# Performance work log

Measured on AMD Instinct MI355X. Metric: run time of the kernel, lower is better.

## Reference

```python
import jax, jax.numpy as jnp
import numpy as np

B, T, D, S, K = 4, 4096, 1024, 2048, 4
LN_EPS = 1e-5


def setup_inputs() -> dict:
    key = jax.random.key(0)
    ks = jax.random.split(key, 9)
    scale = 0.02
    return {
        "x": jax.random.normal(ks[0], (B, T, D), jnp.float32),
        "W_in": jax.random.normal(ks[1], (D, 2 * S), jnp.float32) * scale,
        "b_in": jnp.zeros((2 * S,), jnp.float32),
        "conv_w": jax.random.normal(ks[2], (S, 1, K), jnp.float32) * scale,  # depthwise [out_ch, in_ch/groups=1, K]
        "conv_b": jnp.zeros((S,), jnp.float32),
        "W_out": jax.random.normal(ks[3], (S, D), jnp.float32) * scale,
        "b_out": jnp.zeros((D,), jnp.float32),
        "gamma": jnp.ones((D,), jnp.float32),
        "beta": jnp.zeros((D,), jnp.float32),
    }


def reference(x, W_in, b_in, conv_w, conv_b, W_out, b_out, gamma, beta):
    # x: [B, T, D]
    residual = x
    proj = x @ W_in + b_in                      # [B, T, 2S]
    mixed, gate = jnp.split(proj, 2, axis=-1)   # each [B, T, S]
    mixed = mixed * jax.nn.sigmoid(gate)
    h = jnp.transpose(mixed, (0, 2, 1))         # [B, S, T]
    k = conv_w.shape[-1]
    # torch pads both sides by K-1 then slices [:T] -> equivalent to causal left-pad K-1
    y = jax.lax.conv_general_dilated(
        h, conv_w,
        window_strides=(1,),
        padding=[(k - 1, 0)],
        dimension_numbers=("NCH", "OIH", "NCH"),
        feature_group_count=conv_w.shape[0],
    ) + conv_b[None, :, None]                   # [B, S, T]
    y = jnp.transpose(y, (0, 2, 1))             # [B, T, S]
    y = y @ W_out + b_out                       # [B, T, D]
    z = residual + y                            # dropout p=0.0 -> identity
    mu = jnp.mean(z, axis=-1, keepdims=True)
    var = jnp.var(z, axis=-1, keepdims=True)
    zn = (z - mu) * jax.lax.rsqrt(var + LN_EPS)
    return zn * gamma + beta
```

## Files before the change

kernel.cpp:

```cpp
#include <hip/hip_runtime.h>
#include <hip/hip_bf16.h>


#define Bdim 4
#define Tdim 4096
#define Ddim 1024
#define Sdim 2048
#define Mdim (Bdim * Tdim)
#define LN_EPS 1e-5f

typedef __bf16 bf16;
typedef __bf16 bf16x8 __attribute__((ext_vector_type(8)));
typedef float f32x4 __attribute__((ext_vector_type(4)));

__device__ __forceinline__ void gload_lds16(const bf16* g, bf16* l) {
  __builtin_amdgcn_global_load_lds((const __attribute__((address_space(1))) void*)g,
                                   (__attribute__((address_space(3))) void*)l,
                                   16, 0, 0);
}

__device__ __forceinline__ f32x4 zero4() {
  f32x4 z; z[0] = 0.f; z[1] = 0.f; z[2] = 0.f; z[3] = 0.f; return z;
}

__global__ __launch_bounds__(256) void k_cast_x(const float* __restrict__ x,
                                                bf16* __restrict__ xb) {
  int gid = blockIdx.x * 256 + threadIdx.x;
  const float4* p = (const float4*)x + (size_t)gid * 2;
  float4 a = p[0], b = p[1];
  bf16x8 o;
  o[0] = (bf16)a.x; o[1] = (bf16)a.y; o[2] = (bf16)a.z; o[3] = (bf16)a.w;
  o[4] = (bf16)b.x; o[5] = (bf16)b.y; o[6] = (bf16)b.z; o[7] = (bf16)b.w;
  ((bf16x8*)xb)[gid] = o;
}

__global__ __launch_bounds__(256) void k_transpose_cast(const float* __restrict__ in,
                                                        bf16* __restrict__ out,
                                                        int R, int C) {
  __shared__ float tile[32][33];
  int tx = threadIdx.x & 31;
  int ty = threadIdx.x >> 5;
  int r0 = blockIdx.y * 32;
  int c0 = blockIdx.x * 32;
#pragma unroll
  for (int i = 0; i < 4; ++i)
    tile[ty + i * 8][tx] = in[(size_t)(r0 + ty + i * 8) * C + c0 + tx];
  __syncthreads();
#pragma unroll
  for (int i = 0; i < 4; ++i)
    out[(size_t)(c0 + ty + i * 8) * R + r0 + tx] = (bf16)tile[tx][ty + i * 8];
}

__global__ __launch_bounds__(256, 2)
void k_gemm1_gate(const bf16* __restrict__ xb, const bf16* __restrict__ wt,
                  const float* __restrict__ b_in, bf16* __restrict__ mixed) {
  __shared__ bf16 Als[128 * 32];
  __shared__ bf16 Bml[128 * 32];
  __shared__ bf16 Bgl[128 * 32];

  const int tid = threadIdx.x;
  const int wave = tid >> 6;
  const int lane = tid & 63;
  const int lr = lane & 15;
  const int lk = lane >> 4;
  const int wr = wave >> 1, wc = wave & 1;

  const int m0 = blockIdx.y * 128;
  const int n0 = blockIdx.x * 128;

  const int srow = lane >> 2;
  const int skoff = (lane & 3) * 8;

  f32x4 accm[4][4], accg[4][4];
#pragma unroll
  for (int i = 0; i < 4; ++i)
#pragma unroll
    for (int j = 0; j < 4; ++j) { accm[i][j] = zero4(); accg[i][j] = zero4(); }

  const bf16* Ag = xb + (size_t)m0 * Ddim;
  const bf16* Bmg = wt + (size_t)n0 * Ddim;
  const bf16* Bgg = wt + (size_t)(Sdim + n0) * Ddim;

  for (int k0 = 0; k0 < Ddim; k0 += 32) {
    __syncthreads();
#pragma unroll
    for (int j = 0; j < 2; ++j) {
      int row = j * 64 + wave * 16 + srow;
      size_t goff = (size_t)row * Ddim + k0 + skoff;
      int lbase = (j * 64 + wave * 16) * 32;
      gload_lds16(Ag + goff, &Als[lbase]);
      gload_lds16(Bmg + goff, &Bml[lbase]);
      gload_lds16(Bgg + goff, &Bgl[lbase]);
    }
    __syncthreads();

    bf16x8 af[4], bmf[4], bgf[4];
#pragma unroll
    for (int mi = 0; mi < 4; ++mi)
      af[mi] = *(const bf16x8*)&Als[(wr * 64 + mi * 16 + lr) * 32 + lk * 8];
#pragma unroll
    for (int ni = 0; ni < 4; ++ni) {
      bmf[ni] = *(const bf16x8*)&Bml[(wc * 64 + ni * 16 + lr) * 32 + lk * 8];
      bgf[ni] = *(const bf16x8*)&Bgl[(wc * 64 + ni * 16 + lr) * 32 + lk * 8];
    }
#pragma unroll
    for (int mi = 0; mi < 4; ++mi)
#pragma unroll
      for (int ni = 0; ni < 4; ++ni) {
        accm[mi][ni] = __builtin_amdgcn_mfma_f32_16x16x32_bf16(af[mi], bmf[ni], accm[mi][ni], 0, 0, 0);
        accg[mi][ni] = __builtin_amdgcn_mfma_f32_16x16x32_bf16(af[mi], bgf[ni], accg[mi][ni], 0, 0, 0);
      }
  }

#pragma unroll
  for (int mi = 0; mi < 4; ++mi)
#pragma unroll
    for (int ni = 0; ni < 4; ++ni)
#pragma unroll
      for (int i = 0; i < 4; ++i) {
        int row = m0 + wr * 64 + mi * 16 + lk * 4 + i;
        int col = n0 + wc * 64 + ni * 16 + lr;
        float pm = accm[mi][ni][i] + b_in[col];
        float pg = accg[mi][ni][i] + b_in[col + Sdim];
        float v = pm / (1.0f + __expf(-pg));
        mixed[(size_t)row * Sdim + col] = (bf16)v;
      }
}

__global__ __launch_bounds__(256) void k_conv(const bf16* __restrict__ mixed,
                                              const float* __restrict__ cw,
                                              const float* __restrict__ cb,
                                              bf16* __restrict__ h) {
  int gid = blockIdx.x * 256 + threadIdx.x;
  int cg = gid & 255;
  int tg = (gid >> 8) & 511;
  int b = gid >> 17;
  int ch0 = cg * 8;
  int t0 = tg * 8;
  const size_t base = ((size_t)b * Tdim) * Sdim + ch0;

  float4 w4[8];
  float bias[8];
#pragma unroll
  for (int j = 0; j < 8; ++j) {
    w4[j] = ((const float4*)cw)[ch0 + j];
    bias[j] = cb[ch0 + j];
  }

  bf16x8 zv;
#pragma unroll
  for (int j = 0; j < 8; ++j) zv[j] = (bf16)0.0f;

  bf16x8 win[11];
#pragma unroll
  for (int i = 0; i < 11; ++i) {
    int t = t0 - 3 + i;
    win[i] = (t >= 0) ? *(const bf16x8*)(mixed + base + (size_t)t * Sdim) : zv;
  }

#pragma unroll
  for (int i = 0; i < 8; ++i) {
    bf16x8 o;
#pragma unroll
    for (int j = 0; j < 8; ++j) {
      float a = bias[j]
              + w4[j].x * (float)win[i + 0][j]
              + w4[j].y * (float)win[i + 1][j]
              + w4[j].z * (float)win[i + 2][j]
              + w4[j].w * (float)win[i + 3][j];
      o[j] = (bf16)a;
    }
    *(bf16x8*)(h + base + (size_t)(t0 + i) * Sdim) = o;
  }
}

__global__ __launch_bounds__(256, 2)
void k_gemm2_res(const bf16* __restrict__ h, const bf16* __restrict__ wt,
                 const float* __restrict__ b_out, const float* __restrict__ x,
                 float* __restrict__ z) {
  __shared__ bf16 Als[128 * 32];
  __shared__ bf16 Bls[128 * 32];

  const int tid = threadIdx.x;
  const int wave = tid >> 6;
  const int lane = tid & 63;
  const int lr = lane & 15;
  const int lk = lane >> 4;
  const int wr = wave >> 1, wc = wave & 1;

  const int m0 = blockIdx.y * 128;
  const int n0 = blockIdx.x * 128;

  const int srow = lane >> 2;
  const int skoff = (lane & 3) * 8;

  f32x4 acc[4][4];
#pragma unroll
  for (int i = 0; i < 4; ++i)
#pragma unroll
    for (int j = 0; j < 4; ++j) acc[i][j] = zero4();

  const bf16* Ag = h + (size_t)m0 * Sdim;
  const bf16* Bg = wt + (size_t)n0 * Sdim;

  for (int k0 = 0; k0 < Sdim; k0 += 32) {
    __syncthreads();
#pragma unroll
    for (int j = 0; j < 2; ++j) {
      int row = j * 64 + wave * 16 + srow;
      size_t goff = (size_t)row * Sdim + k0 + skoff;
      int lbase = (j * 64 + wave * 16) * 32;
      gload_lds16(Ag + goff, &Als[lbase]);
      gload_lds16(Bg + goff, &Bls[lbase]);
    }
    __syncthreads();

    bf16x8 af[4], bf[4];
#pragma unroll
    for (int mi = 0; mi < 4; ++mi)
      af[mi] = *(const bf16x8*)&Als[(wr * 64 + mi * 16 + lr) * 32 + lk * 8];
#pragma unroll
    for (int ni = 0; ni < 4; ++ni)
      bf[ni] = *(const bf16x8*)&Bls[(wc * 64 + ni * 16 + lr) * 32 + lk * 8];
#pragma unroll
    for (int mi = 0; mi < 4; ++mi)
#pragma unroll
      for (int ni = 0; ni < 4; ++ni)
        acc[mi][ni] = __builtin_amdgcn_mfma_f32_16x16x32_bf16(af[mi], bf[ni], acc[mi][ni], 0, 0, 0);
  }

#pragma unroll
  for (int mi = 0; mi < 4; ++mi)
#pragma unroll
    for (int ni = 0; ni < 4; ++ni)
#pragma unroll
      for (int i = 0; i < 4; ++i) {
        int row = m0 + wr * 64 + mi * 16 + lk * 4 + i;
        int col = n0 + wc * 64 + ni * 16 + lr;
        size_t idx = (size_t)row * Ddim + col;
        z[idx] = x[idx] + b_out[col] + acc[mi][ni][i];
      }
}

__global__ __launch_bounds__(256) void k_ln(const float* __restrict__ z,
                                            const float* __restrict__ gamma,
                                            const float* __restrict__ beta,
                                            float* __restrict__ out) {
  int row = blockIdx.x;
  int tid = threadIdx.x;
  const float4* zr = (const float4*)(z + (size_t)row * Ddim);
  float4 v = zr[tid];
  float s = v.x + v.y + v.z + v.w;
  float ss = v.x * v.x + v.y * v.y + v.z * v.z + v.w * v.w;
#pragma unroll
  for (int off = 32; off > 0; off >>= 1) {
    s += __shfl_xor(s, off);
    ss += __shfl_xor(ss, off);
  }
  __shared__ float ps[4], pss[4];
  int wave = tid >> 6, lane = tid & 63;
  if (lane == 0) { ps[wave] = s; pss[wave] = ss; }
  __syncthreads();
  float tots = ps[0] + ps[1] + ps[2] + ps[3];
  float totss = pss[0] + pss[1] + pss[2] + pss[3];
  float mu = tots * (1.0f / (float)Ddim);
  float var = totss * (1.0f / (float)Ddim) - mu * mu;
  float rs = rsqrtf(var + LN_EPS);
  float4 gg = ((const float4*)gamma)[tid];
  float4 bb = ((const float4*)beta)[tid];
  float4 o;
  o.x = (v.x - mu) * rs * gg.x + bb.x;
  o.y = (v.y - mu) * rs * gg.y + bb.y;
  o.z = (v.z - mu) * rs * gg.z + bb.z;
  o.w = (v.w - mu) * rs * gg.w + bb.w;
  ((float4*)(out + (size_t)row * Ddim))[tid] = o;
}

extern "C" void kernel_launch(void* const* d_in, const int* in_sizes, int n_in,
                              void* d_out, int out_size, void* d_ws, size_t ws_size,
                              hipStream_t stream) {
  const float* x = (const float*)d_in[0];
  const float* W_in = (const float*)d_in[1];
  const float* b_in = (const float*)d_in[2];
  const float* conv_w = (const float*)d_in[3];
  const float* conv_b = (const float*)d_in[4];
  const float* W_out = (const float*)d_in[5];
  const float* b_out = (const float*)d_in[6];
  const float* gamma = (const float*)d_in[7];
  const float* beta = (const float*)d_in[8];
  float* out = (float*)d_out;

  char* ws = (char*)d_ws;
  bf16* mixed = (bf16*)ws;
  bf16* hbuf = (bf16*)(ws + ((size_t)64 << 20));
  bf16* xb = (bf16*)(ws + ((size_t)128 << 20));
  bf16* winT = (bf16*)(ws + ((size_t)160 << 20));
  bf16* woutT = (bf16*)(ws + ((size_t)168 << 20));
  float* z = (float*)mixed;

  k_cast_x<<<dim3(Mdim * Ddim / 8 / 256), dim3(256), 0, stream>>>(x, xb);
  k_transpose_cast<<<dim3(4096 / 32, 1024 / 32), dim3(256), 0, stream>>>(W_in, winT, 1024, 4096);
  k_transpose_cast<<<dim3(1024 / 32, 2048 / 32), dim3(256), 0, stream>>>(W_out, woutT, 2048, 1024);
  k_gemm1_gate<<<dim3(Sdim / 128, Mdim / 128), dim3(256), 0, stream>>>(xb, winT, b_in, mixed);
  k_conv<<<dim3(Bdim * (Tdim / 8) * (Sdim / 8) / 256), dim3(256), 0, stream>>>(mixed, conv_w, conv_b, hbuf);
  k_gemm2_res<<<dim3(Ddim / 128, Mdim / 128), dim3(256), 0, stream>>>(hbuf, woutT, b_out, x, z);
  k_ln<<<dim3(Mdim), dim3(256), 0, stream>>>(z, gamma, beta, out);
}
```

Before: 443.7 us.

## Replace both GEMMs with a 256x256 double-buffered, swizzled, barrier-scheduled MFMA kernel

```diff
diff --git a/kernel.cpp b/kernel.cpp
--- a/kernel.cpp
+++ b/kernel.cpp
@@ -12,6 +12,12 @@
 typedef __bf16 bf16;
 typedef __bf16 bf16x8 __attribute__((ext_vector_type(8)));
 typedef float f32x4 __attribute__((ext_vector_type(4)));
+
+#define BAR() __builtin_amdgcn_s_barrier()
+#define SCHED() __builtin_amdgcn_sched_barrier(0)
+#define LGKM0() asm volatile("s_waitcnt lgkmcnt(0)" ::: "memory")
+#define VMCNT4() asm volatile("s_waitcnt vmcnt(4)" ::: "memory")
+#define VMCNT0() asm volatile("s_waitcnt vmcnt(0)" ::: "memory")
 
 __device__ __forceinline__ void gload_lds16(const bf16* g, bf16* l) {
   __builtin_amdgcn_global_load_lds((const __attribute__((address_space(1))) void*)g,
@@ -36,7 +42,7 @@
 
 __global__ __launch_bounds__(256) void k_transpose_cast(const float* __restrict__ in,
                                                         bf16* __restrict__ out,
-                                                        int R, int C) {
+                                                        int R, int C, int permmode) {
   __shared__ float tile[32][33];
   int tx = threadIdx.x & 31;
   int ty = threadIdx.x >> 5;
@@ -47,84 +53,191 @@
     tile[ty + i * 8][tx] = in[(size_t)(r0 + ty + i * 8) * C + c0 + tx];
   __syncthreads();
 #pragma unroll
-  for (int i = 0; i < 4; ++i)
-    out[(size_t)(c0 + ty + i * 8) * R + r0 + tx] = (bf16)tile[tx][ty + i * 8];
-}
-
-__global__ __launch_bounds__(256, 2)
-void k_gemm1_gate(const bf16* __restrict__ xb, const bf16* __restrict__ wt,
-                  const float* __restrict__ b_in, bf16* __restrict__ mixed) {
-  __shared__ bf16 Als[128 * 32];
-  __shared__ bf16 Bml[128 * 32];
-  __shared__ bf16 Bgl[128 * 32];
+  for (int i = 0; i < 4; ++i) {
+    int oc = c0 + ty + i * 8;
+    int pr = oc;
+    if (permmode) {
+      pr = (oc < 2048) ? ((oc >> 4) * 32 + (oc & 15))
+                       : (((oc - 2048) >> 4) * 32 + 16 + (oc & 15));
+    }
+    out[(size_t)pr * R + r0 + tx] = (bf16)tile[tx][ty + i * 8];
+  }
+}
+
+template<int KTOT, int NTN, int EPI>
+__global__ __launch_bounds__(512, 1)
+void k_gemm256(const bf16* __restrict__ Ag, const bf16* __restrict__ Bg,
+               const float* __restrict__ bias, const float* __restrict__ xres,
+               bf16* __restrict__ outb, float* __restrict__ outf) {
+  __shared__ __attribute__((aligned(16))) char lds[131072];
 
   const int tid = threadIdx.x;
-  const int wave = tid >> 6;
-  const int lane = tid & 63;
-  const int lr = lane & 15;
-  const int lk = lane >> 4;
-  const int wr = wave >> 1, wc = wave & 1;
-
-  const int m0 = blockIdx.y * 128;
-  const int n0 = blockIdx.x * 128;
-
-  const int srow = lane >> 2;
-  const int skoff = (lane & 3) * 8;
-
-  f32x4 accm[4][4], accg[4][4];
-#pragma unroll
-  for (int i = 0; i < 4; ++i)
-#pragma unroll
-    for (int j = 0; j < 4; ++j) { accm[i][j] = zero4(); accg[i][j] = zero4(); }
-
-  const bf16* Ag = xb + (size_t)m0 * Ddim;
-  const bf16* Bmg = wt + (size_t)n0 * Ddim;
-  const bf16* Bgg = wt + (size_t)(Sdim + n0) * Ddim;
-
-  for (int k0 = 0; k0 < Ddim; k0 += 32) {
-    __syncthreads();
-#pragma unroll
-    for (int j = 0; j < 2; ++j) {
-      int row = j * 64 + wave * 16 + srow;
-      size_t goff = (size_t)row * Ddim + k0 + skoff;
-      int lbase = (j * 64 + wave * 16) * 32;
-      gload_lds16(Ag + goff, &Als[lbase]);
-      gload_lds16(Bmg + goff, &Bml[lbase]);
-      gload_lds16(Bgg + goff, &Bgl[lbase]);
-    }
-    __syncthreads();
-
-    bf16x8 af[4], bmf[4], bgf[4];
-#pragma unroll
-    for (int mi = 0; mi < 4; ++mi)
-      af[mi] = *(const bf16x8*)&Als[(wr * 64 + mi * 16 + lr) * 32 + lk * 8];
-#pragma unroll
-    for (int ni = 0; ni < 4; ++ni) {
-      bmf[ni] = *(const bf16x8*)&Bml[(wc * 64 + ni * 16 + lr) * 32 + lk * 8];
-      bgf[ni] = *(const bf16x8*)&Bgl[(wc * 64 + ni * 16 + lr) * 32 + lk * 8];
-    }
-#pragma unroll
-    for (int mi = 0; mi < 4; ++mi)
-#pragma unroll
-      for (int ni = 0; ni < 4; ++ni) {
-        accm[mi][ni] = __builtin_amdgcn_mfma_f32_16x16x32_bf16(af[mi], bmf[ni], accm[mi][ni], 0, 0, 0);
-        accg[mi][ni] = __builtin_amdgcn_mfma_f32_16x16x32_bf16(af[mi], bgf[ni], accg[mi][ni], 0, 0, 0);
-      }
-  }
-
-#pragma unroll
-  for (int mi = 0; mi < 4; ++mi)
-#pragma unroll
-    for (int ni = 0; ni < 4; ++ni)
-#pragma unroll
-      for (int i = 0; i < 4; ++i) {
-        int row = m0 + wr * 64 + mi * 16 + lk * 4 + i;
-        int col = n0 + wc * 64 + ni * 16 + lr;
-        float pm = accm[mi][ni][i] + b_in[col];
-        float pg = accg[mi][ni][i] + b_in[col + Sdim];
-        float v = pm / (1.0f + __expf(-pg));
-        mixed[(size_t)row * Sdim + col] = (bf16)v;
-      }
+  const int w = tid >> 6, lane = tid & 63;
+  const int lr = lane & 15, lk = lane >> 4;
+  const int wr = w >> 2, wc = w & 3;
+
+  const int nwg = gridDim.x;
+  const int bid = blockIdx.x;
+  const int wg = (bid & 7) * (nwg >> 3) + (bid >> 3);
+  const int m0 = (wg / NTN) * 256;
+  const int n0 = (wg % NTN) * 256;
+
+  const int lsw = (lane * 16) ^ (((lane >> 5) & 1) << 5);
+  const int rw = lsw >> 7;
+  const int cw = (lsw & 127) >> 1;
+
+  const int xorm = ((lr >> 2) & 1) << 5;
+  const int aoff = (lr * 128 + lk * 16) ^ xorm;
+  const int boff = ((((wc & 1) * 64 + lr) * 128) + lk * 16) ^ xorm;
+  const char* ldsA = lds + wr * 16384;
+  const char* ldsB = lds + 32768 + (wc >> 1) * 16384;
+
+  auto stage = [&](const bf16* G, int row0, int kt, int regionByte) {
+#pragma unroll
+    for (int L = 0; L < 2; ++L) {
+      int q = w * 2 + L;
+      const bf16* src = G + (size_t)(row0 + q * 8 + rw) * KTOT + kt * 64 + cw;
+      gload_lds16(src, (bf16*)(lds + regionByte + q * 1024));
+    }
+  };
+  auto rdA = [&](int s, int mi, int ks) -> bf16x8 {
+    return *(const bf16x8*)(ldsA + s * 65536 + mi * 2048 + ks * 64 + aoff);
+  };
+  auto rdB = [&](int s, int nj, int ks) -> bf16x8 {
+    return *(const bf16x8*)(ldsB + s * 65536 + nj * 2048 + ks * 64 + boff);
+  };
+
+  f32x4 acc[8][4];
+#pragma unroll
+  for (int i = 0; i < 8; ++i)
+#pragma unroll
+    for (int j = 0; j < 4; ++j) acc[i][j] = zero4();
+
+  bf16x8 a[4][2], b[4][2];
+
+#define QUAD(rh, ch)                                                                   \
+  {                                                                                    \
+    _Pragma("unroll")                                                                  \
+    for (int mi = 0; mi < 4; ++mi) {                                                   \
+      _Pragma("unroll")                                                                \
+      for (int nj = 0; nj < 2; ++nj) {                                                 \
+        acc[(rh)*4+mi][(ch)*2+nj] = __builtin_amdgcn_mfma_f32_16x16x32_bf16(           \
+            a[mi][0], b[(ch)*2+nj][0], acc[(rh)*4+mi][(ch)*2+nj], 0, 0, 0);            \
+        acc[(rh)*4+mi][(ch)*2+nj] = __builtin_amdgcn_mfma_f32_16x16x32_bf16(           \
+            a[mi][1], b[(ch)*2+nj][1], acc[(rh)*4+mi][(ch)*2+nj], 0, 0, 0);            \
+      }                                                                                \
+    }                                                                                  \
+  }
+
+  const int NI = KTOT / 128;
+
+  stage(Bg, n0,       0, 32768);
+  stage(Bg, n0 + 128, 0, 32768 + 16384);
+  stage(Ag, m0,       0, 0);
+  stage(Ag, m0 + 128, 0, 16384);
+  stage(Bg, n0,       1, 65536 + 32768);
+  stage(Bg, n0 + 128, 1, 65536 + 32768 + 16384);
+  VMCNT4(); SCHED(); BAR(); SCHED();
+
+  for (int i = 0; i < NI; ++i) {
+    const int kta2 = 2 * i + 2;
+    const int ktb  = 2 * i + 1;
+    const bool nl = (i < NI - 1);
+
+#pragma unroll
+    for (int mi = 0; mi < 4; ++mi) { a[mi][0] = rdA(0, mi, 0); a[mi][1] = rdA(0, mi, 1); }
+#pragma unroll
+    for (int nj = 0; nj < 2; ++nj) { b[nj][0] = rdB(0, nj, 0); b[nj][1] = rdB(0, nj, 1); }
+    stage(Ag, m0, ktb, 65536);
+    asm volatile("s_waitcnt lgkmcnt(8)" ::: "memory");
+    SCHED(); BAR(); LGKM0(); SCHED();
+    __builtin_amdgcn_s_setprio(1); QUAD(0, 0); __builtin_amdgcn_s_setprio(0);
+    SCHED(); BAR(); SCHED();
+
+#pragma unroll
+    for (int nj = 0; nj < 2; ++nj) { b[2+nj][0] = rdB(0, 2+nj, 0); b[2+nj][1] = rdB(0, 2+nj, 1); }
+    stage(Ag, m0 + 128, ktb, 65536 + 16384);
+    SCHED(); BAR(); LGKM0(); SCHED();
+    __builtin_amdgcn_s_setprio(1); QUAD(0, 1); __builtin_amdgcn_s_setprio(0);
+    SCHED(); BAR(); SCHED();
+
+#pragma unroll
+    for (int mi = 0; mi < 4; ++mi) { a[mi][0] = rdA(0, 4+mi, 0); a[mi][1] = rdA(0, 4+mi, 1); }
+    if (nl) stage(Bg, n0, kta2, 32768);
+    SCHED(); BAR(); LGKM0(); SCHED();
+    __builtin_amdgcn_s_setprio(1); QUAD(1, 0); __builtin_amdgcn_s_setprio(0);
+    SCHED(); BAR(); SCHED();
+
+    if (nl) stage(Bg, n0 + 128, kta2, 32768 + 16384);
+    SCHED(); BAR(); LGKM0(); SCHED();
+    __builtin_amdgcn_s_setprio(1); QUAD(1, 1); __builtin_amdgcn_s_setprio(0);
+    if (nl) { VMCNT4(); } else { VMCNT0(); }
+    SCHED(); BAR(); SCHED();
+
+#pragma unroll
+    for (int mi = 0; mi < 4; ++mi) { a[mi][0] = rdA(1, mi, 0); a[mi][1] = rdA(1, mi, 1); }
+#pragma unroll
+    for (int nj = 0; nj < 2; ++nj) { b[nj][0] = rdB(1, nj, 0); b[nj][1] = rdB(1, nj, 1); }
+    if (nl) stage(Ag, m0, kta2, 0);
+    asm volatile("s_waitcnt lgkmcnt(8)" ::: "memory");
+    SCHED(); BAR(); LGKM0(); SCHED();
+    __builtin_amdgcn_s_setprio(1); QUAD(0, 0); __builtin_amdgcn_s_setprio(0);
+    SCHED(); BAR(); SCHED();
+
+#pragma unroll
+    for (int nj = 0; nj < 2; ++nj) { b[2+nj][0] = rdB(1, 2+nj, 0); b[2+nj][1] = rdB(1, 2+nj, 1); }
+    if (nl) stage(Ag, m0 + 128, kta2, 16384);
+    SCHED(); BAR(); LGKM0(); SCHED();
+    __builtin_amdgcn_s_setprio(1); QUAD(0, 1); __builtin_amdgcn_s_setprio(0);
+    SCHED(); BAR(); SCHED();
+
+#pragma unroll
+    for (int mi = 0; mi < 4; ++mi) { a[mi][0] = rdA(1, 4+mi, 0); a[mi][1] = rdA(1, 4+mi, 1); }
+    if (nl) stage(Bg, n0, ktb + 2, 65536 + 32768);
+    SCHED(); BAR(); LGKM0(); SCHED();
+    __builtin_amdgcn_s_setprio(1); QUAD(1, 0); __builtin_amdgcn_s_setprio(0);
+    SCHED(); BAR(); SCHED();
+
+    if (nl) stage(Bg, n0 + 128, ktb + 2, 65536 + 32768 + 16384);
+    SCHED(); BAR(); LGKM0(); SCHED();
+    __builtin_amdgcn_s_setprio(1); QUAD(1, 1); __builtin_amdgcn_s_setprio(0);
+    if (nl) { VMCNT4(); }
+    SCHED(); BAR(); SCHED();
+  }
+#undef QUAD
+
+  if (EPI == 0) {
+#pragma unroll
+    for (int p = 0; p < 2; ++p) {
+      const int g = (n0 + wc * 64 + p * 32) >> 5;
+      const int mcol = g * 16 + lr;
+      const float bm = bias[mcol];
+      const float bg = bias[mcol + 2048];
+#pragma unroll
+      for (int mi = 0; mi < 8; ++mi)
+#pragma unroll
+        for (int ii = 0; ii < 4; ++ii) {
+          const int row = m0 + wr * 128 + mi * 16 + lk * 4 + ii;
+          const float pm = acc[mi][2 * p][ii] + bm;
+          const float pg = acc[mi][2 * p + 1][ii] + bg;
+          outb[(size_t)row * Sdim + mcol] = (bf16)(pm / (1.0f + __expf(-pg)));
+        }
+    }
+  } else {
+#pragma unroll
+    for (int nj = 0; nj < 4; ++nj) {
+      const int col = n0 + wc * 64 + nj * 16 + lr;
+      const float bo = bias[col];
+#pragma unroll
+      for (int mi = 0; mi < 8; ++mi)
+#pragma unroll
+        for (int ii = 0; ii < 4; ++ii) {
+          const int row = m0 + wr * 128 + mi * 16 + lk * 4 + ii;
+          const size_t idx = (size_t)row * Ddim + col;
+          outf[idx] = xres[idx] + bo + acc[mi][nj][ii];
+        }
+    }
+  }
 }
 
 __global__ __launch_bounds__(256) void k_conv(const bf16* __restrict__ mixed,
@@ -134,10 +247,10 @@
   int gid = blockIdx.x * 256 + threadIdx.x;
   int cg = gid & 255;
   int tg = (gid >> 8) & 511;
-  int b = gid >> 17;
+  int bb = gid >> 17;
   int ch0 = cg * 8;
   int t0 = tg * 8;
-  const size_t base = ((size_t)b * Tdim) * Sdim + ch0;
+  const size_t base = ((size_t)bb * Tdim) * Sdim + ch0;
 
   float4 w4[8];
   float bias[8];
@@ -163,83 +276,15 @@
     bf16x8 o;
 #pragma unroll
     for (int j = 0; j < 8; ++j) {
-      float a = bias[j]
+      float aa = bias[j]
               + w4[j].x * (float)win[i + 0][j]
               + w4[j].y * (float)win[i + 1][j]
               + w4[j].z * (float)win[i + 2][j]
               + w4[j].w * (float)win[i + 3][j];
-      o[j] = (bf16)a;
+      o[j] = (bf16)aa;
     }
     *(bf16x8*)(h + base + (size_t)(t0 + i) * Sdim) = o;
   }
-}
-
-__global__ __launch_bounds__(256, 2)
-void k_gemm2_res(const bf16* __restrict__ h, const bf16* __restrict__ wt,
-                 const float* __restrict__ b_out, const float* __restrict__ x,
-                 float* __restrict__ z) {
-  __shared__ bf16 Als[128 * 32];
-  __shared__ bf16 Bls[128 * 32];
-
-  const int tid = threadIdx.x;
-  const int wave = tid >> 6;
-  const int lane = tid & 63;
-  const int lr = lane & 15;
-  const int lk = lane >> 4;
-  const int wr = wave >> 1, wc = wave & 1;
-
-  const int m0 = blockIdx.y * 128;
-  const int n0 = blockIdx.x * 128;
-
-  const int srow = lane >> 2;
-  const int skoff = (lane & 3) * 8;
-
-  f32x4 acc[4][4];
-#pragma unroll
-  for (int i = 0; i < 4; ++i)
-#pragma unroll
-    for (int j = 0; j < 4; ++j) acc[i][j] = zero4();
-
-  const bf16* Ag = h + (size_t)m0 * Sdim;
-  const bf16* Bg = wt + (size_t)n0 * Sdim;
-
-  for (int k0 = 0; k0 < Sdim; k0 += 32) {
-    __syncthreads();
-#pragma unroll
-    for (int j = 0; j < 2; ++j) {
-      int row = j * 64 + wave * 16 + srow;
-      size_t goff = (size_t)row * Sdim + k0 + skoff;
-      int lbase = (j * 64 + wave * 16) * 32;
-      gload_lds16(Ag + goff, &Als[lbase]);
-      gload_lds16(Bg + goff, &Bls[lbase]);
-    }
-    __syncthreads();
-
-    bf16x8 af[4], bf[4];
-#pragma unroll
-    for (int mi = 0; mi < 4; ++mi)
-      af[mi] = *(const bf16x8*)&Als[(wr * 64 + mi * 16 + lr) * 32 + lk * 8];
-#pragma unroll
-    for (int ni = 0; ni < 4; ++ni)
-      bf[ni] = *(const bf16x8*)&Bls[(wc * 64 + ni * 16 + lr) * 32 + lk * 8];
-#pragma unroll
-    for (int mi = 0; mi < 4; ++mi)
-#pragma unroll
-      for (int ni = 0; ni < 4; ++ni)
-        acc[mi][ni] = __builtin_amdgcn_mfma_f32_16x16x32_bf16(af[mi], bf[ni], acc[mi][ni], 0, 0, 0);
-  }
-
-#pragma unroll
-  for (int mi = 0; mi < 4; ++mi)
-#pragma unroll
-    for (int ni = 0; ni < 4; ++ni)
-#pragma unroll
-      for (int i = 0; i < 4; ++i) {
-        int row = m0 + wr * 64 + mi * 16 + lk * 4 + i;
-        int col = n0 + wc * 64 + ni * 16 + lr;
-        size_t idx = (size_t)row * Ddim + col;
-        z[idx] = x[idx] + b_out[col] + acc[mi][ni][i];
-      }
 }
 
 __global__ __launch_bounds__(256) void k_ln(const float* __restrict__ z,
@@ -299,10 +344,17 @@
   float* z = (float*)mixed;
 
   k_cast_x<<<dim3(Mdim * Ddim / 8 / 256), dim3(256), 0, stream>>>(x, xb);
-  k_transpose_cast<<<dim3(4096 / 32, 1024 / 32), dim3(256), 0, stream>>>(W_in, winT, 1024, 4096);
-  k_transpose_cast<<<dim3(1024 / 32, 2048 / 32), dim3(256), 0, stream>>>(W_out, woutT, 2048, 1024);
-  k_gemm1_gate<<<dim3(Sdim / 128, Mdim / 128), dim3(256), 0, stream>>>(xb, winT, b_in, mixed);
-  k_conv<<<dim3(Bdim * (Tdim / 8) * (Sdim / 8) / 256), dim3(256), 0, stream>>>(mixed, conv_w, conv_b, hbuf);
-  k_gemm2_res<<<dim3(Ddim / 128, Mdim / 128), dim3(256), 0, stream>>>(hbuf, woutT, b_out, x, z);
+  k_transpose_cast<<<dim3(4096 / 32, 1024 / 32), dim3(256), 0, stream>>>(W_in, winT, 1024, 4096, 1);
+  k_transpose_cast<<<dim3(1024 / 32, 2048 / 32), dim3(256), 0, stream>>>(W_out, woutT, 2048, 1024, 0);
+
+  k_gemm256<1024, 16, 0><<<dim3(Mdim / 256 * (4096 / 256)), dim3(512), 0, stream>>>(
+      xb, winT, b_in, nullptr, mixed, nullptr);
+
+  k_conv<<<dim3(Bdim * (Tdim / 8) * (Sdim / 8) / 256), dim3(256), 0, stream>>>(
+      mixed, conv_w, conv_b, hbuf);
+
+  k_gemm256<2048, 4, 1><<<dim3(Mdim / 256 * (Ddim / 256)), dim3(512), 0, stream>>>(
+      hbuf, woutT, b_out, x, nullptr, z);
+
   k_ln<<<dim3(Mdim), dim3(256), 0, stream>>>(z, gamma, beta, out);
 }
```

New measurement: 470.1 us. +6.0%, slower.
